# Optimization experiments

Measured on AMD Instinct MI355X. Metric: run time of the kernel, lower is better.

The kernel has to match this reference:

```python
import jax, jax.numpy as jnp
import numpy as np


def _conv1x1(x, w, b):
    # x: [B,C,H,W], w: [O,C], b: [O] -> [B,O,H,W]
    return jnp.einsum('bchw,oc->bohw', x, w) + b[None, :, None, None]


def setup_inputs() -> dict:
    key = jax.random.key(0)
    ks = jax.random.split(key, 5)
    B, C, H, W = 4, 256, 64, 64
    C2 = C // 2
    scale = 0.02  # keep attention logits in a sane range
    return {
        'x': jax.random.normal(ks[0], (B, C, H, W), dtype=jnp.float32),
        'w_theta': jax.random.normal(ks[1], (C2, C), dtype=jnp.float32) * scale,
        'b_theta': jnp.zeros((C2,), dtype=jnp.float32),
        'w_phi': jax.random.normal(ks[2], (C2, C), dtype=jnp.float32) * scale,
        'b_phi': jnp.zeros((C2,), dtype=jnp.float32),
        'w_g': jax.random.normal(ks[3], (C2, C), dtype=jnp.float32) * scale,
        'b_g': jnp.zeros((C2,), dtype=jnp.float32),
        'w_out': jax.random.normal(ks[4], (C, C2), dtype=jnp.float32) * scale,
        'b_out': jnp.zeros((C,), dtype=jnp.float32),
    }


def reference(x, w_theta, b_theta, w_phi, b_phi, w_g, b_g, w_out, b_out):
    B, C, H, W = x.shape
    C2 = C // 2
    N = H * W
    theta = _conv1x1(x, w_theta, b_theta).reshape(B, C2, N)  # [B,C2,N]
    phi = _conv1x1(x, w_phi, b_phi).reshape(B, C2, N)        # [B,C2,N]
    g = _conv1x1(x, w_g, b_g).reshape(B, C2, N)              # [B,C2,N]
    # non-local attention: scores[b,m,n] = theta[b,:,m] . phi[b,:,n]
    scores = jnp.einsum('bcm,bcn->bmn', theta, phi)          # [B,N,N]
    attn = jax.nn.softmax(scores, axis=-1)                   # [B,N,N]
    # output = g @ attn^T : out[b,c,m] = sum_n g[b,c,n] * attn[b,m,n]
    out = jnp.einsum('bcn,bmn->bcm', g, attn)                # [B,C2,N]
    out = out.reshape(B, C2, H, W)
    return x + _conv1x1(out, w_out, b_out)
```

## Files before the change

kernel.cpp:

```cpp
#include <hip/hip_runtime.h>
#include <hip/hip_bf16.h>

#define B_  4
#define C_  256
#define C2_ 128
#define N_  4096
#define LOG2E 1.4426950408889634f

typedef unsigned short u16;
typedef __attribute__((ext_vector_type(8))) short bf16x8;
typedef __attribute__((ext_vector_type(4))) float f32x4;

static __device__ __forceinline__ u16 f2bf(float f) {
    return __builtin_bit_cast(u16, __float2bfloat16(f));
}
static __device__ __forceinline__ float bf2f(u16 u) {
    return __bfloat162float(__builtin_bit_cast(__hip_bfloat16, u));
}
static __device__ __forceinline__ bf16x8 cvt8(const float* p) {
    u16 t[8];
#pragma unroll
    for (int j = 0; j < 8; ++j) t[j] = f2bf(p[j]);
    return *(const bf16x8*)t;
}

#define XW 264

__global__ __launch_bounds__(256, 2) void projx_kernel(
    const float* __restrict__ x,
    const float* __restrict__ wt, const float* __restrict__ wp,
    const float* __restrict__ wg,
    const float* __restrict__ b_theta, const float* __restrict__ b_phi,
    const float* __restrict__ b_g,
    u16* __restrict__ Q, u16* __restrict__ K, u16* __restrict__ V) {
    __shared__ __align__(16) u16 XTs[64][XW];
    __shared__ __align__(16) u16 Ws[64][XW];
    u16 (*Vt)[72] = (u16(*)[72])XTs;

    int p = blockIdx.x;
    int b = (p & 7) >> 1;
    int j = ((p >> 3) << 1) | (p & 1);
    int h  = j >> 6;
    int n0 = (j & 63) * 64;
    int tid = threadIdx.x;
    int wave = tid >> 6, lane = tid & 63, quad = (lane >> 4) & 3, l16 = lane & 15;

#pragma unroll
    for (int it = 0; it < 8; ++it) {
        int idx = it * 256 + tid;
        int q = idx & 15, pp = idx >> 4;
        const float* r0 = x + ((size_t)b * C_ + 2 * pp) * N_ + n0 + 4 * q;
        float4 v0 = *(const float4*)r0;
        float4 v1 = *(const float4*)(r0 + N_);
        const float* f0 = (const float*)&v0;
        const float* f1 = (const float*)&v1;
#pragma unroll
        for (int jj = 0; jj < 4; ++jj) {
            unsigned pk = (unsigned)f2bf(f0[jj]) | ((unsigned)f2bf(f1[jj]) << 16);
            *(unsigned*)&XTs[4 * q + jj][2 * pp] = pk;
        }
    }
    __syncthreads();

    bf16x8 af[8];
#pragma unroll
    for (int ks = 0; ks < 8; ++ks)
        af[ks] = *(const bf16x8*)&XTs[wave * 16 + l16][ks * 32 + quad * 8];
    __syncthreads();

    const float* wms[3]    = { wt, wp, wg };
    const float* biases[3] = { b_theta, b_phi, b_g };

#pragma unroll
    for (int mat = 0; mat < 3; ++mat) {
        const float* wm = wms[mat];
        const float* bias = biases[mat];
#pragma unroll
        for (int it = 0; it < 8; ++it) {
            int idx = it * 256 + tid;
            int row = idx >> 5, c8 = (idx & 31) * 8;
            const float* src = wm + (size_t)(h * 64 + row) * C_ + c8;
            float w8[8];
            *(float4*)&w8[0] = *(const float4*)src;
            *(float4*)&w8[4] = *(const float4*)(src + 4);
            *(bf16x8*)&Ws[row][c8] = cvt8(w8);
        }
        __syncthreads();

        f32x4 acc[4];
#pragma unroll
        for (int i = 0; i < 4; ++i) acc[i] = (f32x4){0.f, 0.f, 0.f, 0.f};
#pragma unroll
        for (int ct = 0; ct < 4; ++ct)
#pragma unroll
            for (int ks = 0; ks < 8; ++ks) {
                bf16x8 bf = *(const bf16x8*)&Ws[ct * 16 + l16][ks * 32 + quad * 8];
                acc[ct] = __builtin_amdgcn_mfma_f32_16x16x32_bf16(
                    af[ks], bf, acc[ct], 0, 0, 0);
            }

        if (mat < 2) {
            u16* dst = mat == 0 ? Q : K;
            float scl = mat == 0 ? LOG2E : 1.0f;
#pragma unroll
            for (int ct = 0; ct < 4; ++ct) {
                int c2 = h * 64 + ct * 16 + l16;
                float bb = bias[c2];
#pragma unroll
                for (int r = 0; r < 4; ++r) {
                    int n = n0 + wave * 16 + quad * 4 + r;
                    dst[((size_t)b * N_ + n) * C2_ + c2] =
                        f2bf((acc[ct][r] + bb) * scl);
                }
            }
        } else {
#pragma unroll
            for (int ct = 0; ct < 4; ++ct) {
                int c2l = ct * 16 + l16;
                float bb = bias[h * 64 + c2l];
#pragma unroll
                for (int r = 0; r < 4; ++r)
                    Vt[c2l][wave * 16 + quad * 4 + r] = f2bf(acc[ct][r] + bb);
            }
        }
        __syncthreads();
    }

#pragma unroll
    for (int it = 0; it < 2; ++it) {
        int idx = it * 256 + tid;
        int row = idx >> 3, n8 = (idx & 7) * 8;
        *(uint4*)(V + ((size_t)b * C2_ + h * 64 + row) * N_ + n0 + n8) =
            *(const uint4*)&Vt[row][n8];
    }
}

__global__ __launch_bounds__(256, 2) void attn_kernel(
    const u16* __restrict__ Q, const u16* __restrict__ K,
    const u16* __restrict__ V, u16* __restrict__ AO,
    u16* __restrict__ Opb, float* __restrict__ lsum, int nsplit) {
    const int BM = 128, BN = 64, D = C2_;
    int p = blockIdx.x;
    int b = (p & 7) >> 1;
    int j = ((p >> 3) << 1) | (p & 1);
    int s  = j >> 5;
    int m0 = (j & 31) * BM;
    int tid  = threadIdx.x;
    int wave = tid >> 6, lane = tid & 63, quad = (lane >> 4) & 3, l16 = lane & 15;

    __shared__ __align__(16) u16 Ks[BN][D + 8];
    __shared__ __align__(16) u16 Vs[D][BN + 8];
    __shared__ __align__(16) u16 Psb[4][32][BN + 8];
    u16* Ps = &Psb[wave][0][0];

    bf16x8 qf[2][4];
#pragma unroll
    for (int ms = 0; ms < 2; ++ms) {
        const u16* qp = Q + ((size_t)b * N_ + m0 + wave * 32 + ms * 16 + l16) * D;
#pragma unroll
        for (int kk = 0; kk < 4; ++kk)
            qf[ms][kk] = *(const bf16x8*)(qp + kk * 32 + quad * 8);
    }

    float l_r[2][4] = {{0.f, 0.f, 0.f, 0.f}, {0.f, 0.f, 0.f, 0.f}};
    f32x4 o_acc[2][8];
#pragma unroll
    for (int ms = 0; ms < 2; ++ms)
#pragma unroll
        for (int i = 0; i < 8; ++i) o_acc[ms][i] = (f32x4){0.f, 0.f, 0.f, 0.f};

    const int tiles = N_ / BN;
    const int base = tiles / nsplit, rem = tiles % nsplit;
    const int t0 = s * base + (s < rem ? s : rem);
    const int cnt = base + (s < rem ? 1 : 0);
    const int nt0 = t0 * BN, nt1 = (t0 + cnt) * BN;

    for (int nt = nt0; nt < nt1; nt += BN) {
        const u16* kp = K + ((size_t)b * N_ + nt) * D;
#pragma unroll
        for (int it = 0; it < 4; ++it) {
            int idx = it * 256 + tid;
            int row = idx >> 4, col = (idx & 15) * 8;
            *(uint4*)&Ks[row][col] = *(const uint4*)(kp + row * D + col);
        }
#pragma unroll
        for (int it = 0; it < 4; ++it) {
            int idx = it * 256 + tid;
            int row = idx >> 3, col = (idx & 7) * 8;
            *(uint4*)&Vs[row][col] =
                *(const uint4*)(V + ((size_t)b * C2_ + row) * N_ + nt + col);
        }
        __syncthreads();

        f32x4 sc[2][4];
#pragma unroll
        for (int nn = 0; nn < 4; ++nn) {
            f32x4 a0 = (f32x4){0.f, 0.f, 0.f, 0.f};
            f32x4 a1 = (f32x4){0.f, 0.f, 0.f, 0.f};
#pragma unroll
            for (int kk = 0; kk < 4; ++kk) {
                bf16x8 kf = *(const bf16x8*)&Ks[nn * 16 + l16][kk * 32 + quad * 8];
                a0 = __builtin_amdgcn_mfma_f32_16x16x32_bf16(qf[0][kk], kf, a0, 0, 0, 0);
                a1 = __builtin_amdgcn_mfma_f32_16x16x32_bf16(qf[1][kk], kf, a1, 0, 0, 0);
            }
            sc[0][nn] = a0;
            sc[1][nn] = a1;
        }

#pragma unroll
        for (int ms = 0; ms < 2; ++ms)
#pragma unroll
            for (int nn = 0; nn < 4; ++nn)
#pragma unroll
                for (int r = 0; r < 4; ++r) {
                    float pv = __builtin_amdgcn_exp2f(sc[ms][nn][r]);
                    l_r[ms][r] += pv;
                    Ps[(ms * 16 + quad * 4 + r) * (BN + 8) + nn * 16 + l16] = f2bf(pv);
                }

#pragma unroll
        for (int ks = 0; ks < 2; ++ks) {
            bf16x8 pf0 = *(const bf16x8*)&Ps[(l16) * (BN + 8) + ks * 32 + quad * 8];
            bf16x8 pf1 = *(const bf16x8*)&Ps[(16 + l16) * (BN + 8) + ks * 32 + quad * 8];
#pragma unroll
            for (int cs = 0; cs < 8; ++cs) {
                bf16x8 vf = *(const bf16x8*)&Vs[cs * 16 + l16][ks * 32 + quad * 8];
                o_acc[0][cs] = __builtin_amdgcn_mfma_f32_16x16x32_bf16(pf0, vf, o_acc[0][cs], 0, 0, 0);
                o_acc[1][cs] = __builtin_amdgcn_mfma_f32_16x16x32_bf16(pf1, vf, o_acc[1][cs], 0, 0, 0);
            }
        }
        __syncthreads();
    }

#pragma unroll
    for (int ms = 0; ms < 2; ++ms)
#pragma unroll
        for (int r = 0; r < 4; ++r) {
            l_r[ms][r] += __shfl_xor(l_r[ms][r], 1);
            l_r[ms][r] += __shfl_xor(l_r[ms][r], 2);
            l_r[ms][r] += __shfl_xor(l_r[ms][r], 4);
            l_r[ms][r] += __shfl_xor(l_r[ms][r], 8);
        }

    if (Opb) {
#pragma unroll
        for (int ms = 0; ms < 2; ++ms) {
#pragma unroll
            for (int cs = 0; cs < 8; ++cs)
#pragma unroll
                for (int r = 0; r < 4; ++r) {
                    size_t row = (size_t)s * (B_ * N_) + (size_t)b * N_ +
                                 m0 + wave * 32 + ms * 16 + quad * 4 + r;
                    Opb[row * C2_ + cs * 16 + l16] = f2bf(o_acc[ms][cs][r]);
                }
            if (l16 == 0)
#pragma unroll
                for (int r = 0; r < 4; ++r) {
                    size_t row = (size_t)s * (B_ * N_) + (size_t)b * N_ +
                                 m0 + wave * 32 + ms * 16 + quad * 4 + r;
                    lsum[row] = l_r[ms][r];
                }
        }
    } else {
#pragma unroll
        for (int ms = 0; ms < 2; ++ms)
#pragma unroll
            for (int cs = 0; cs < 8; ++cs)
#pragma unroll
                for (int r = 0; r < 4; ++r) {
                    float v = o_acc[ms][cs][r] / l_r[ms][r];
                    AO[((size_t)b * N_ + m0 + wave * 32 + ms * 16 + quad * 4 + r) * C2_ +
                       cs * 16 + l16] = f2bf(v);
                }
    }
}

#define OW 136

__global__ __launch_bounds__(256, 4) void outproj_kernel(
    const float* __restrict__ x, const u16* __restrict__ Opb,
    const float* __restrict__ lsum, const u16* __restrict__ AO,
    const float* __restrict__ w_out, const float* __restrict__ b_out,
    float* __restrict__ y, int nsplit) {
    __shared__ __align__(16) u16 As[64][OW];
    __shared__ __align__(16) u16 Ws2[64][OW];
    __shared__ float Ls[64];
    float (*Yt)[68] = (float(*)[68])&As[0][0];

    int p = blockIdx.x;
    int b = (p & 7) >> 1;
    int j = ((p >> 3) << 1) | (p & 1);
    int c0 = (j >> 6) * 64;
    int n0 = (j & 63) * 64;
    int tid = threadIdx.x;
    int wave = tid >> 6, lane = tid & 63, quad = (lane >> 4) & 3, l16 = lane & 15;

#pragma unroll
    for (int it = 0; it < 4; ++it) {
        int idx = it * 256 + tid;
        int row = idx >> 4, c8 = (idx & 15) * 8;
        const float* src = w_out + (size_t)(c0 + row) * C2_ + c8;
        float w8[8];
        *(float4*)&w8[0] = *(const float4*)src;
        *(float4*)&w8[4] = *(const float4*)(src + 4);
        *(bf16x8*)&Ws2[row][c8] = cvt8(w8);
    }

    if (nsplit > 1) {
        if (tid < 64) {
            float L = 0.f;
            for (int s = 0; s < nsplit; ++s)
                L += lsum[(size_t)s * (B_ * N_) + (size_t)b * N_ + n0 + tid];
            Ls[tid] = 1.f / L;
        }
        __syncthreads();
#pragma unroll
        for (int it = 0; it < 4; ++it) {
            int idx = it * 256 + tid;
            int n = idx >> 4, c8 = (idx & 15) * 8;
            float a[8] = {0.f, 0.f, 0.f, 0.f, 0.f, 0.f, 0.f, 0.f};
            for (int s = 0; s < nsplit; ++s) {
                const u16* op = Opb +
                    ((size_t)s * (B_ * N_) + (size_t)b * N_ + n0 + n) * C2_ + c8;
                uint4 raw = *(const uint4*)op;
                const u16* rp = (const u16*)&raw;
#pragma unroll
                for (int jj = 0; jj < 8; ++jj) a[jj] += bf2f(rp[jj]);
            }
            float inv = Ls[n];
            u16 o[8];
#pragma unroll
            for (int jj = 0; jj < 8; ++jj) o[jj] = f2bf(a[jj] * inv);
            *(uint4*)&As[n][c8] = *(const uint4*)o;
        }
    } else {
#pragma unroll
        for (int it = 0; it < 4; ++it) {
            int idx = it * 256 + tid;
            int n = idx >> 4, c8 = (idx & 15) * 8;
            *(uint4*)&As[n][c8] =
                *(const uint4*)(AO + ((size_t)b * N_ + n0 + n) * C2_ + c8);
        }
    }
    __syncthreads();

    bf16x8 af[4];
#pragma unroll
    for (int kk = 0; kk < 4; ++kk)
        af[kk] = *(const bf16x8*)&Ws2[wave * 16 + l16][kk * 32 + quad * 8];

    f32x4 acc[4];
#pragma unroll
    for (int i = 0; i < 4; ++i) acc[i] = (f32x4){0.f, 0.f, 0.f, 0.f};

#pragma unroll
    for (int nn = 0; nn < 4; ++nn)
#pragma unroll
        for (int kk = 0; kk < 4; ++kk) {
            bf16x8 bf = *(const bf16x8*)&As[nn * 16 + l16][kk * 32 + quad * 8];
            acc[nn] = __builtin_amdgcn_mfma_f32_16x16x32_bf16(af[kk], bf, acc[nn], 0, 0, 0);
        }

    int cw = c0 + wave * 16;
    float bo[4];
#pragma unroll
    for (int r = 0; r < 4; ++r) bo[r] = b_out[cw + quad * 4 + r];

    __syncthreads();
#pragma unroll
    for (int nn = 0; nn < 4; ++nn)
#pragma unroll
        for (int r = 0; r < 4; ++r)
            Yt[wave * 16 + quad * 4 + r][nn * 16 + l16] = acc[nn][r] + bo[r];
    __syncthreads();

    {
        int row = tid >> 2, sg = (tid & 3) * 16;
        const float4* xr = (const float4*)(x + ((size_t)b * C_ + c0 + row) * N_ + n0 + sg);
        float4*       yr = (float4*)(y + ((size_t)b * C_ + c0 + row) * N_ + n0 + sg);
        const float4* tr = (const float4*)&Yt[row][sg];
#pragma unroll
        for (int jj = 0; jj < 4; ++jj) {
            float4 xv = xr[jj];
            float4 tv = tr[jj];
            yr[jj] = make_float4(xv.x + tv.x, xv.y + tv.y,
                                 xv.z + tv.z, xv.w + tv.w);
        }
    }
}

extern "C" void kernel_launch(void* const* d_in, const int* in_sizes, int n_in,
                              void* d_out, int out_size, void* d_ws, size_t ws_size,
                              hipStream_t stream) {
    const float* x       = (const float*)d_in[0];
    const float* w_theta = (const float*)d_in[1];
    const float* b_theta = (const float*)d_in[2];
    const float* w_phi   = (const float*)d_in[3];
    const float* b_phi   = (const float*)d_in[4];
    const float* w_g     = (const float*)d_in[5];
    const float* b_g     = (const float*)d_in[6];
    const float* w_out   = (const float*)d_in[7];
    const float* b_out   = (const float*)d_in[8];
    float* y = (float*)d_out;

    const size_t SZ = (size_t)B_ * N_ * C2_;
    u16* Q = (u16*)d_ws;
    u16* K = Q + SZ;
    u16* V = K + SZ;
    char* dyn = (char*)(V + SZ);
    size_t fixedB = 3 * SZ * 2;

    size_t perS = SZ * 2 + (size_t)B_ * N_ * 4;

    int S;
    if      (ws_size >= fixedB + 4 * perS) S = 4;
    else if (ws_size >= fixedB + 2 * perS) S = 2;
    else                                   S = 1;

    u16*   AO  = (u16*)dyn;
    u16*   Opb = nullptr;
    float* ls  = nullptr;
    if (S > 1) {
        Opb = (u16*)dyn;
        ls  = (float*)(Opb + (size_t)S * SZ);
    }

    projx_kernel<<<B_ * (N_ / 64) * 2, 256, 0, stream>>>(
        x, w_theta, w_phi, w_g, b_theta, b_phi, b_g, Q, K, V);
    attn_kernel<<<B_ * (N_ / 128) * S, 256, 0, stream>>>(Q, K, V, AO, Opb, ls, S);
    outproj_kernel<<<B_ * (C_ / 64) * (N_ / 64), 256, 0, stream>>>(
        x, Opb, ls, AO, w_out, b_out, y, S);
}
```

Measured before the change: 156.3 us.

## Prefetch next K/V tile into registers and coalesce Q/K projection stores

The attention loop now loads the next K and V tiles into registers while the current tile's QK and PV MFMAs run, then writes them to shared memory after a barrier. This hides global-load latency behind compute, at the cost of more registers and an extra barrier per tile. The projection kernel also stages Q and K outputs through shared memory so they are written with 16-byte coalesced stores instead of scattered 2-byte stores.

```diff
diff --git a/kernel.cpp b/kernel.cpp
--- a/kernel.cpp
+++ b/kernel.cpp
@@ -100,38 +100,35 @@
             }
 
         if (mat < 2) {
-            u16* dst = mat == 0 ? Q : K;
             float scl = mat == 0 ? LOG2E : 1.0f;
-#pragma unroll
-            for (int ct = 0; ct < 4; ++ct) {
-                int c2 = h * 64 + ct * 16 + l16;
-                float bb = bias[c2];
-#pragma unroll
-                for (int r = 0; r < 4; ++r) {
-                    int n = n0 + wave * 16 + quad * 4 + r;
-                    dst[((size_t)b * N_ + n) * C2_ + c2] =
-                        f2bf((acc[ct][r] + bb) * scl);
-                }
-            }
-        } else {
 #pragma unroll
             for (int ct = 0; ct < 4; ++ct) {
                 int c2l = ct * 16 + l16;
                 float bb = bias[h * 64 + c2l];
 #pragma unroll
                 for (int r = 0; r < 4; ++r)
+                    Vt[wave * 16 + quad * 4 + r][c2l] =
+                        f2bf((acc[ct][r] + bb) * scl);
+            }
+            __syncthreads();
+            u16* dst = mat == 0 ? Q : K;
+            int row = tid >> 3, c8 = (tid & 7) * 8;
+            *(uint4*)(dst + ((size_t)b * N_ + n0 + row) * C2_ + h * 64 + c8) =
+                *(const uint4*)&Vt[row][c8];
+        } else {
+#pragma unroll
+            for (int ct = 0; ct < 4; ++ct) {
+                int c2l = ct * 16 + l16;
+                float bb = bias[h * 64 + c2l];
+#pragma unroll
+                for (int r = 0; r < 4; ++r)
                     Vt[c2l][wave * 16 + quad * 4 + r] = f2bf(acc[ct][r] + bb);
             }
-        }
-        __syncthreads();
-    }
-
-#pragma unroll
-    for (int it = 0; it < 2; ++it) {
-        int idx = it * 256 + tid;
-        int row = idx >> 3, n8 = (idx & 7) * 8;
-        *(uint4*)(V + ((size_t)b * C2_ + h * 64 + row) * N_ + n0 + n8) =
-            *(const uint4*)&Vt[row][n8];
+            __syncthreads();
+            int row = tid >> 3, n8 = (tid & 7) * 8;
+            *(uint4*)(V + ((size_t)b * C2_ + h * 64 + row) * N_ + n0 + n8) =
+                *(const uint4*)&Vt[row][n8];
+        }
     }
 }
 
@@ -175,22 +172,50 @@
     const int cnt = base + (s < rem ? 1 : 0);
     const int nt0 = t0 * BN, nt1 = (t0 + cnt) * BN;
 
+    const u16* kbase = K + (size_t)b * N_ * D;
+    const u16* vbase = V + (size_t)b * C2_ * N_;
+
+    uint4 kpre[4], vpre[4];
+#pragma unroll
+    for (int it = 0; it < 4; ++it) {
+        int idx = it * 256 + tid;
+        kpre[it] = *(const uint4*)(kbase + (size_t)(nt0 + (idx >> 4)) * D +
+                                   (idx & 15) * 8);
+    }
+#pragma unroll
+    for (int it = 0; it < 4; ++it) {
+        int idx = it * 256 + tid;
+        vpre[it] = *(const uint4*)(vbase + (size_t)(idx >> 3) * N_ + nt0 +
+                                   (idx & 7) * 8);
+    }
+#pragma unroll
+    for (int it = 0; it < 4; ++it) {
+        int idx = it * 256 + tid;
+        *(uint4*)&Ks[idx >> 4][(idx & 15) * 8] = kpre[it];
+    }
+#pragma unroll
+    for (int it = 0; it < 4; ++it) {
+        int idx = it * 256 + tid;
+        *(uint4*)&Vs[idx >> 3][(idx & 7) * 8] = vpre[it];
+    }
+    __syncthreads();
+
     for (int nt = nt0; nt < nt1; nt += BN) {
-        const u16* kp = K + ((size_t)b * N_ + nt) * D;
-#pragma unroll
-        for (int it = 0; it < 4; ++it) {
-            int idx = it * 256 + tid;
-            int row = idx >> 4, col = (idx & 15) * 8;
-            *(uint4*)&Ks[row][col] = *(const uint4*)(kp + row * D + col);
-        }
-#pragma unroll
-        for (int it = 0; it < 4; ++it) {
-            int idx = it * 256 + tid;
-            int row = idx >> 3, col = (idx & 7) * 8;
-            *(uint4*)&Vs[row][col] =
-                *(const uint4*)(V + ((size_t)b * C2_ + row) * N_ + nt + col);
-        }
-        __syncthreads();
+        bool pf = (nt + BN) < nt1;
+        if (pf) {
+#pragma unroll
+            for (int it = 0; it < 4; ++it) {
+                int idx = it * 256 + tid;
+                kpre[it] = *(const uint4*)(kbase +
+                    (size_t)(nt + BN + (idx >> 4)) * D + (idx & 15) * 8);
+            }
+#pragma unroll
+            for (int it = 0; it < 4; ++it) {
+                int idx = it * 256 + tid;
+                vpre[it] = *(const uint4*)(vbase +
+                    (size_t)(idx >> 3) * N_ + nt + BN + (idx & 7) * 8);
+            }
+        }
 
         f32x4 sc[2][4];
 #pragma unroll
@@ -227,6 +252,20 @@
                 bf16x8 vf = *(const bf16x8*)&Vs[cs * 16 + l16][ks * 32 + quad * 8];
                 o_acc[0][cs] = __builtin_amdgcn_mfma_f32_16x16x32_bf16(pf0, vf, o_acc[0][cs], 0, 0, 0);
                 o_acc[1][cs] = __builtin_amdgcn_mfma_f32_16x16x32_bf16(pf1, vf, o_acc[1][cs], 0, 0, 0);
+            }
+        }
+        __syncthreads();
+
+        if (pf) {
+#pragma unroll
+            for (int it = 0; it < 4; ++it) {
+                int idx = it * 256 + tid;
+                *(uint4*)&Ks[idx >> 4][(idx & 15) * 8] = kpre[it];
+            }
+#pragma unroll
+            for (int it = 0; it < 4; ++it) {
+                int idx = it * 256 + tid;
+                *(uint4*)&Vs[idx >> 3][(idx & 7) * 8] = vpre[it];
             }
         }
         __syncthreads();
```

New measurement: 198.7 us. +27.1%, slower.

## Load K/V fragments directly from global memory and allow eight-way key split

Applied to the files above, without the earlier changes.

The attention kernel no longer stages K and V tiles into shared memory behind block-wide barriers. Each wave now reads its MFMA operand fragments straight from global memory, and the softmax exponentials are fused into the per-subtile score loop. This removes the LDS staging traffic and both __syncthreads per tile, but each of the four waves now fetches the same K/V data separately, so the kernel relies on L1/L2 hits and its V reads are strided. The host also allows a split count of 8 when workspace permits, giving more blocks at the cost of a larger partial-sum combine.

```diff
diff --git a/kernel.cpp b/kernel.cpp
--- a/kernel.cpp
+++ b/kernel.cpp
@@ -148,8 +148,6 @@
     int tid  = threadIdx.x;
     int wave = tid >> 6, lane = tid & 63, quad = (lane >> 4) & 3, l16 = lane & 15;
 
-    __shared__ __align__(16) u16 Ks[BN][D + 8];
-    __shared__ __align__(16) u16 Vs[D][BN + 8];
     __shared__ __align__(16) u16 Psb[4][32][BN + 8];
     u16* Ps = &Psb[wave][0][0];
 
@@ -175,61 +173,47 @@
     const int cnt = base + (s < rem ? 1 : 0);
     const int nt0 = t0 * BN, nt1 = (t0 + cnt) * BN;
 
+    const u16* kb_lane = K + ((size_t)b * N_ + l16) * D + quad * 8;
+    const u16* vb_lane = V + ((size_t)b * C2_ + l16) * N_ + quad * 8;
+
     for (int nt = nt0; nt < nt1; nt += BN) {
-        const u16* kp = K + ((size_t)b * N_ + nt) * D;
-#pragma unroll
-        for (int it = 0; it < 4; ++it) {
-            int idx = it * 256 + tid;
-            int row = idx >> 4, col = (idx & 15) * 8;
-            *(uint4*)&Ks[row][col] = *(const uint4*)(kp + row * D + col);
-        }
-#pragma unroll
-        for (int it = 0; it < 4; ++it) {
-            int idx = it * 256 + tid;
-            int row = idx >> 3, col = (idx & 7) * 8;
-            *(uint4*)&Vs[row][col] =
-                *(const uint4*)(V + ((size_t)b * C2_ + row) * N_ + nt + col);
-        }
-        __syncthreads();
-
-        f32x4 sc[2][4];
 #pragma unroll
         for (int nn = 0; nn < 4; ++nn) {
+            const u16* kp = kb_lane + (size_t)(nt + nn * 16) * D;
+            bf16x8 kf[4];
+#pragma unroll
+            for (int kk = 0; kk < 4; ++kk)
+                kf[kk] = *(const bf16x8*)(kp + kk * 32);
             f32x4 a0 = (f32x4){0.f, 0.f, 0.f, 0.f};
             f32x4 a1 = (f32x4){0.f, 0.f, 0.f, 0.f};
 #pragma unroll
             for (int kk = 0; kk < 4; ++kk) {
-                bf16x8 kf = *(const bf16x8*)&Ks[nn * 16 + l16][kk * 32 + quad * 8];
-                a0 = __builtin_amdgcn_mfma_f32_16x16x32_bf16(qf[0][kk], kf, a0, 0, 0, 0);
-                a1 = __builtin_amdgcn_mfma_f32_16x16x32_bf16(qf[1][kk], kf, a1, 0, 0, 0);
-            }
-            sc[0][nn] = a0;
-            sc[1][nn] = a1;
-        }
-
-#pragma unroll
-        for (int ms = 0; ms < 2; ++ms)
-#pragma unroll
-            for (int nn = 0; nn < 4; ++nn)
-#pragma unroll
-                for (int r = 0; r < 4; ++r) {
-                    float pv = __builtin_amdgcn_exp2f(sc[ms][nn][r]);
-                    l_r[ms][r] += pv;
-                    Ps[(ms * 16 + quad * 4 + r) * (BN + 8) + nn * 16 + l16] = f2bf(pv);
-                }
+                a0 = __builtin_amdgcn_mfma_f32_16x16x32_bf16(qf[0][kk], kf[kk], a0, 0, 0, 0);
+                a1 = __builtin_amdgcn_mfma_f32_16x16x32_bf16(qf[1][kk], kf[kk], a1, 0, 0, 0);
+            }
+#pragma unroll
+            for (int r = 0; r < 4; ++r) {
+                float p0 = __builtin_amdgcn_exp2f(a0[r]);
+                float p1 = __builtin_amdgcn_exp2f(a1[r]);
+                l_r[0][r] += p0;
+                l_r[1][r] += p1;
+                Ps[(quad * 4 + r) * (BN + 8) + nn * 16 + l16]      = f2bf(p0);
+                Ps[(16 + quad * 4 + r) * (BN + 8) + nn * 16 + l16] = f2bf(p1);
+            }
+        }
 
 #pragma unroll
         for (int ks = 0; ks < 2; ++ks) {
             bf16x8 pf0 = *(const bf16x8*)&Ps[(l16) * (BN + 8) + ks * 32 + quad * 8];
             bf16x8 pf1 = *(const bf16x8*)&Ps[(16 + l16) * (BN + 8) + ks * 32 + quad * 8];
+            const u16* vp = vb_lane + nt + ks * 32;
 #pragma unroll
             for (int cs = 0; cs < 8; ++cs) {
-                bf16x8 vf = *(const bf16x8*)&Vs[cs * 16 + l16][ks * 32 + quad * 8];
+                bf16x8 vf = *(const bf16x8*)(vp + (size_t)cs * 16 * N_);
                 o_acc[0][cs] = __builtin_amdgcn_mfma_f32_16x16x32_bf16(pf0, vf, o_acc[0][cs], 0, 0, 0);
                 o_acc[1][cs] = __builtin_amdgcn_mfma_f32_16x16x32_bf16(pf1, vf, o_acc[1][cs], 0, 0, 0);
             }
         }
-        __syncthreads();
     }
 
 #pragma unroll
@@ -413,7 +397,8 @@
     size_t perS = SZ * 2 + (size_t)B_ * N_ * 4;
 
     int S;
-    if      (ws_size >= fixedB + 4 * perS) S = 4;
+    if      (ws_size >= fixedB + 8 * perS) S = 8;
+    else if (ws_size >= fixedB + 4 * perS) S = 4;
     else if (ws_size >= fixedB + 2 * perS) S = 2;
     else                                   S = 1;
 
```

New measurement: 248.8 us. 59.2% more time.

## Switch attention to 32x32x16 MFMA with transposed scores kept in registers

Applied to the files above, without the earlier changes.

Rewrites the attention inner loop to use 32x32x16 bf16 MFMA. Scores are computed as K·Q^T, so the exponentiated probabilities land directly in the register layout the PV MFMA expects as its B operand, and the per-wave shared-memory round trip for P is removed. The V tile is stored in shared memory with a permuted column layout to match. Output is staged through shared memory to get coalesced 16-byte global stores. Row sums reduce with a single shuffle instead of four. The cost is a larger accumulator footprint and a more delicate layout mapping, which raises register pressure under launch_bounds(256,2).

```diff
diff --git a/kernel.cpp b/kernel.cpp
--- a/kernel.cpp
+++ b/kernel.cpp
@@ -10,6 +10,8 @@
 typedef unsigned short u16;
 typedef __attribute__((ext_vector_type(8))) short bf16x8;
 typedef __attribute__((ext_vector_type(4))) float f32x4;
+typedef __attribute__((ext_vector_type(16))) float f32x16;
+typedef __attribute__((ext_vector_type(4))) unsigned u32x4;
 
 static __device__ __forceinline__ u16 f2bf(float f) {
     return __builtin_bit_cast(u16, __float2bfloat16(f));
@@ -146,28 +148,27 @@
     int s  = j >> 5;
     int m0 = (j & 31) * BM;
     int tid  = threadIdx.x;
-    int wave = tid >> 6, lane = tid & 63, quad = (lane >> 4) & 3, l16 = lane & 15;
-
-    __shared__ __align__(16) u16 Ks[BN][D + 8];
-    __shared__ __align__(16) u16 Vs[D][BN + 8];
-    __shared__ __align__(16) u16 Psb[4][32][BN + 8];
-    u16* Ps = &Psb[wave][0][0];
-
-    bf16x8 qf[2][4];
-#pragma unroll
-    for (int ms = 0; ms < 2; ++ms) {
-        const u16* qp = Q + ((size_t)b * N_ + m0 + wave * 32 + ms * 16 + l16) * D;
-#pragma unroll
-        for (int kk = 0; kk < 4; ++kk)
-            qf[ms][kk] = *(const bf16x8*)(qp + kk * 32 + quad * 8);
-    }
-
-    float l_r[2][4] = {{0.f, 0.f, 0.f, 0.f}, {0.f, 0.f, 0.f, 0.f}};
-    f32x4 o_acc[2][8];
-#pragma unroll
-    for (int ms = 0; ms < 2; ++ms)
-#pragma unroll
-        for (int i = 0; i < 8; ++i) o_acc[ms][i] = (f32x4){0.f, 0.f, 0.f, 0.f};
+    int wave = tid >> 6, lane = tid & 63;
+    int l32 = lane & 31, hi8 = (lane >> 5) * 8, hi4 = (lane >> 5) * 4;
+
+    __shared__ __align__(16) u16 Ks[64][136];
+    __shared__ __align__(16) u16 Vs[128][72];
+    __shared__ __align__(16) u16 Ob[4][32][136];
+
+    bf16x8 qf[8];
+    {
+        const u16* qp = Q + ((size_t)b * N_ + m0 + wave * 32 + l32) * D + hi8;
+#pragma unroll
+        for (int c = 0; c < 8; ++c)
+            qf[c] = *(const bf16x8*)(qp + c * 16);
+    }
+
+    float l_r = 0.f;
+    f32x16 o_acc[4];
+#pragma unroll
+    for (int i = 0; i < 4; ++i)
+#pragma unroll
+        for (int r = 0; r < 16; ++r) o_acc[i][r] = 0.f;
 
     const int tiles = N_ / BN;
     const int base = tiles / nsplit, rem = tiles % nsplit;
@@ -187,91 +188,78 @@
         for (int it = 0; it < 4; ++it) {
             int idx = it * 256 + tid;
             int row = idx >> 3, col = (idx & 7) * 8;
-            *(uint4*)&Vs[row][col] =
-                *(const uint4*)(V + ((size_t)b * C2_ + row) * N_ + nt + col);
+            uint4 raw = *(const uint4*)(V + ((size_t)b * C2_ + row) * N_ + nt + col);
+            int dst = (col & ~15) + ((col & 8) >> 1);
+            *(uint2*)&Vs[row][dst]     = make_uint2(raw.x, raw.y);
+            *(uint2*)&Vs[row][dst + 8] = make_uint2(raw.z, raw.w);
         }
         __syncthreads();
 
-        f32x4 sc[2][4];
-#pragma unroll
-        for (int nn = 0; nn < 4; ++nn) {
-            f32x4 a0 = (f32x4){0.f, 0.f, 0.f, 0.f};
-            f32x4 a1 = (f32x4){0.f, 0.f, 0.f, 0.f};
-#pragma unroll
-            for (int kk = 0; kk < 4; ++kk) {
-                bf16x8 kf = *(const bf16x8*)&Ks[nn * 16 + l16][kk * 32 + quad * 8];
-                a0 = __builtin_amdgcn_mfma_f32_16x16x32_bf16(qf[0][kk], kf, a0, 0, 0, 0);
-                a1 = __builtin_amdgcn_mfma_f32_16x16x32_bf16(qf[1][kk], kf, a1, 0, 0, 0);
+        f32x16 sc0, sc1;
+#pragma unroll
+        for (int r = 0; r < 16; ++r) { sc0[r] = 0.f; sc1[r] = 0.f; }
+#pragma unroll
+        for (int c = 0; c < 8; ++c) {
+            bf16x8 kf0 = *(const bf16x8*)&Ks[l32][c * 16 + hi8];
+            bf16x8 kf1 = *(const bf16x8*)&Ks[32 + l32][c * 16 + hi8];
+            sc0 = __builtin_amdgcn_mfma_f32_32x32x16_bf16(kf0, qf[c], sc0, 0, 0, 0);
+            sc1 = __builtin_amdgcn_mfma_f32_32x32x16_bf16(kf1, qf[c], sc1, 0, 0, 0);
+        }
+
+        unsigned w0[8], w1[8];
+#pragma unroll
+        for (int t = 0; t < 8; ++t) {
+            float a0 = __builtin_amdgcn_exp2f(sc0[2 * t]);
+            float a1 = __builtin_amdgcn_exp2f(sc0[2 * t + 1]);
+            float b0 = __builtin_amdgcn_exp2f(sc1[2 * t]);
+            float b1 = __builtin_amdgcn_exp2f(sc1[2 * t + 1]);
+            l_r += (a0 + a1) + (b0 + b1);
+            w0[t] = (unsigned)f2bf(a0) | ((unsigned)f2bf(a1) << 16);
+            w1[t] = (unsigned)f2bf(b0) | ((unsigned)f2bf(b1) << 16);
+        }
+        bf16x8 pf[4];
+        pf[0] = __builtin_bit_cast(bf16x8, (u32x4){w0[0], w0[1], w0[2], w0[3]});
+        pf[1] = __builtin_bit_cast(bf16x8, (u32x4){w0[4], w0[5], w0[6], w0[7]});
+        pf[2] = __builtin_bit_cast(bf16x8, (u32x4){w1[0], w1[1], w1[2], w1[3]});
+        pf[3] = __builtin_bit_cast(bf16x8, (u32x4){w1[4], w1[5], w1[6], w1[7]});
+
+#pragma unroll
+        for (int c = 0; c < 4; ++c)
+#pragma unroll
+            for (int dblk = 0; dblk < 4; ++dblk) {
+                bf16x8 vf = *(const bf16x8*)&Vs[dblk * 32 + l32][c * 16 + hi8];
+                o_acc[dblk] = __builtin_amdgcn_mfma_f32_32x32x16_bf16(
+                    vf, pf[c], o_acc[dblk], 0, 0, 0);
             }
-            sc[0][nn] = a0;
-            sc[1][nn] = a1;
-        }
-
-#pragma unroll
-        for (int ms = 0; ms < 2; ++ms)
-#pragma unroll
-            for (int nn = 0; nn < 4; ++nn)
-#pragma unroll
-                for (int r = 0; r < 4; ++r) {
-                    float pv = __builtin_amdgcn_exp2f(sc[ms][nn][r]);
-                    l_r[ms][r] += pv;
-                    Ps[(ms * 16 + quad * 4 + r) * (BN + 8) + nn * 16 + l16] = f2bf(pv);
-                }
-
-#pragma unroll
-        for (int ks = 0; ks < 2; ++ks) {
-            bf16x8 pf0 = *(const bf16x8*)&Ps[(l16) * (BN + 8) + ks * 32 + quad * 8];
-            bf16x8 pf1 = *(const bf16x8*)&Ps[(16 + l16) * (BN + 8) + ks * 32 + quad * 8];
-#pragma unroll
-            for (int cs = 0; cs < 8; ++cs) {
-                bf16x8 vf = *(const bf16x8*)&Vs[cs * 16 + l16][ks * 32 + quad * 8];
-                o_acc[0][cs] = __builtin_amdgcn_mfma_f32_16x16x32_bf16(pf0, vf, o_acc[0][cs], 0, 0, 0);
-                o_acc[1][cs] = __builtin_amdgcn_mfma_f32_16x16x32_bf16(pf1, vf, o_acc[1][cs], 0, 0, 0);
-            }
-        }
         __syncthreads();
     }
 
-#pragma unroll
-    for (int ms = 0; ms < 2; ++ms)
-#pragma unroll
-        for (int r = 0; r < 4; ++r) {
-            l_r[ms][r] += __shfl_xor(l_r[ms][r], 1);
-            l_r[ms][r] += __shfl_xor(l_r[ms][r], 2);
-            l_r[ms][r] += __shfl_xor(l_r[ms][r], 4);
-            l_r[ms][r] += __shfl_xor(l_r[ms][r], 8);
-        }
-
+    float l_tot = l_r + __shfl_xor(l_r, 32);
+    float scale = Opb ? 1.0f : 1.0f / l_tot;
+
+#pragma unroll
+    for (int dblk = 0; dblk < 4; ++dblk)
+#pragma unroll
+        for (int r = 0; r < 16; ++r) {
+            int d = dblk * 32 + (r & 3) + 8 * (r >> 2) + hi4;
+            Ob[wave][l32][d] = f2bf(o_acc[dblk][r] * scale);
+        }
+
+    int mloc = lane >> 1, half = lane & 1;
     if (Opb) {
-#pragma unroll
-        for (int ms = 0; ms < 2; ++ms) {
-#pragma unroll
-            for (int cs = 0; cs < 8; ++cs)
-#pragma unroll
-                for (int r = 0; r < 4; ++r) {
-                    size_t row = (size_t)s * (B_ * N_) + (size_t)b * N_ +
-                                 m0 + wave * 32 + ms * 16 + quad * 4 + r;
-                    Opb[row * C2_ + cs * 16 + l16] = f2bf(o_acc[ms][cs][r]);
-                }
-            if (l16 == 0)
-#pragma unroll
-                for (int r = 0; r < 4; ++r) {
-                    size_t row = (size_t)s * (B_ * N_) + (size_t)b * N_ +
-                                 m0 + wave * 32 + ms * 16 + quad * 4 + r;
-                    lsum[row] = l_r[ms][r];
-                }
-        }
+        size_t row = (size_t)s * (B_ * N_) + (size_t)b * N_ + m0 + wave * 32 + mloc;
+#pragma unroll
+        for (int k = 0; k < 8; ++k)
+            *(uint4*)(Opb + row * C2_ + half * 64 + k * 8) =
+                *(const uint4*)&Ob[wave][mloc][half * 64 + k * 8];
+        if (lane < 32)
+            lsum[(size_t)s * (B_ * N_) + (size_t)b * N_ + m0 + wave * 32 + lane] = l_tot;
     } else {
-#pragma unroll
-        for (int ms = 0; ms < 2; ++ms)
-#pragma unroll
-            for (int cs = 0; cs < 8; ++cs)
-#pragma unroll
-                for (int r = 0; r < 4; ++r) {
-                    float v = o_acc[ms][cs][r] / l_r[ms][r];
-                    AO[((size_t)b * N_ + m0 + wave * 32 + ms * 16 + quad * 4 + r) * C2_ +
-                       cs * 16 + l16] = f2bf(v);
-                }
+        size_t row = (size_t)b * N_ + m0 + wave * 32 + mloc;
+#pragma unroll
+        for (int k = 0; k < 8; ++k)
+            *(uint4*)(AO + row * C2_ + half * 64 + k * 8) =
+                *(const uint4*)&Ob[wave][mloc][half * 64 + k * 8];
     }
 }
 
```

New measurement: 149.6 us. 1.04x faster.
